# Performance work log

Measured on AMD Instinct MI355X. Metric: run time of the kernel, lower is better.

The kernel has to match this reference:

```python
import jax, jax.numpy as jnp
import numpy as np

HEAD_SIZE = 64

def setup_inputs() -> dict:
    key = jax.random.key(0)
    k1, k2, k3, k4 = jax.random.split(key, 4)
    B, T, C = 4, 4096, 768
    s = 1.0 / np.sqrt(C)
    return {
        "x": jax.random.normal(k1, (B, T, C), dtype=jnp.float32),
        "Wq": jax.random.normal(k2, (C, HEAD_SIZE), dtype=jnp.float32) * s,
        "Wk": jax.random.normal(k3, (C, HEAD_SIZE), dtype=jnp.float32) * s,
        "Wv": jax.random.normal(k4, (C, HEAD_SIZE), dtype=jnp.float32) * s,
    }

def reference(x, Wq, Wk, Wv):
    # x: [B,T,C]; Wq/Wk/Wv: [C,H]
    T = x.shape[1]
    q = jnp.einsum('btc,ch->bth', x, Wq)
    k = jnp.einsum('btc,ch->bth', x, Wk)
    v = jnp.einsum('btc,ch->bth', x, Wv)
    scale = HEAD_SIZE ** (-0.5)
    wei = jnp.einsum('bth,bsh->bts', q, k) * scale  # [B,T,T]
    causal = jnp.tril(jnp.ones((T, T), dtype=bool))
    wei = jnp.where(causal, wei, -jnp.inf)
    wei = jax.nn.softmax(wei, axis=-1)
    # dropout p=0.0 -> identity
    out = jnp.einsum('bts,bsh->bth', wei, v)  # [B,T,H]
    return out
```

## Files before the change

### kernel.cpp

```cpp
#include <hip/hip_runtime.h>
#include <hip/hip_bf16.h>
#include <stdint.h>

typedef unsigned short u16;
typedef __attribute__((ext_vector_type(8))) __bf16 bf16x8;
typedef __attribute__((ext_vector_type(4))) float f32x4;

#define LOG2E 1.44269504088896340736f

__device__ inline u16 f2bf(float f){
  uint32_t u = __float_as_uint(f);
  u += 0x7FFFu + ((u >> 16) & 1u);
  return (u16)(u >> 16);
}
__device__ inline float bf2f(u16 v){
  return __uint_as_float(((uint32_t)v) << 16);
}

__global__ __launch_bounds__(256) void wt_kernel(const float* __restrict__ Wq,
                                                 const float* __restrict__ Wk,
                                                 const float* __restrict__ Wv,
                                                 u16* __restrict__ wtf){
  int idx = blockIdx.x * 256 + threadIdx.x;
  if (idx >= 192 * 768) return;
  int n = idx / 768, c = idx - n * 768;
  int h = n & 63;
  const float* W = (n < 64) ? Wq : ((n < 128) ? Wk : Wv);
  float v = W[c * 64 + h];
  if (n < 64) v *= 0.125f * LOG2E;
  int f = n >> 4, n16 = n & 15;
  int kstep = c >> 5, quad = (c >> 3) & 3, j = c & 7;
  wtf[(size_t)((f * 24 + kstep) * 64 + quad * 16 + n16) * 8 + j] = f2bf(v);
}

__global__ __launch_bounds__(256) void proj_kernel(const float* __restrict__ x,
                                                   const u16* __restrict__ wtf,
                                                   u16* __restrict__ qs,
                                                   u16* __restrict__ ksf,
                                                   u16* __restrict__ vtf){
  __shared__ u16 At[24 * 64 * 8];
  const int tid = threadIdx.x;
  const int w = tid >> 6, lane = tid & 63;
  const int n16 = lane & 15, quad = lane >> 4;
  const int rt = blockIdx.x * 16;

  const float* xb = x + (size_t)rt * 768;
  float4 t[12];
#pragma unroll
  for (int i = 0; i < 12; ++i)
    t[i] = *(const float4*)(xb + (size_t)(i * 256 + tid) * 4);
#pragma unroll
  for (int i = 0; i < 12; ++i){
    int l = i * 256 + tid;
    int row = l / 192, c4 = l - row * 192;
    int ksn = c4 >> 3, qd = (c4 >> 1) & 3, j0 = (c4 & 1) * 4;
    int idx = ((ksn * 64 + qd * 16 + row) * 8 + j0) ^ ((ksn & 7) << 3);
    union { ushort4 s; u16 e[4]; } pk;
    pk.e[0] = f2bf(t[i].x); pk.e[1] = f2bf(t[i].y);
    pk.e[2] = f2bf(t[i].z); pk.e[3] = f2bf(t[i].w);
    *(ushort4*)&At[idx] = pk.s;
  }
  __syncthreads();

  const f32x4 fz = {0.f, 0.f, 0.f, 0.f};
  f32x4 acc[3];
#pragma unroll
  for (int j = 0; j < 3; ++j) acc[j] = fz;

#pragma unroll
  for (int kst = 0; kst < 24; ++kst){
    const int sw = (kst & 7) << 3;
    bf16x8 a = *(const bf16x8*)&At[((kst * 64 + lane) * 8) ^ sw];
#pragma unroll
    for (int j = 0; j < 3; ++j){
      bf16x8 bfr = *(const bf16x8*)(wtf + (size_t)(((3 * w + j) * 24 + kst) * 64 + lane) * 8);
      acc[j] = __builtin_amdgcn_mfma_f32_16x16x32_bf16(a, bfr, acc[j], 0, 0, 0);
    }
  }
  __syncthreads();

#pragma unroll
  for (int j = 0; j < 3; ++j){
    const int F = 3 * w + j;
    const int s = F >> 2, c0 = (F & 3) * 16;
#pragma unroll
    for (int r = 0; r < 4; ++r){
      u16 val = f2bf(acc[j][r]);
      int row = quad * 4 + r;
      if (s < 2) At[s * 1152 + row * 72 + c0 + n16] = val;
      else       At[2304 + (c0 + n16) * 24 + row]   = val;
    }
  }
  __syncthreads();

  const int bb = rt >> 12, t0 = rt & 4095;
  const int kt = t0 >> 6;
  const int fk = (t0 >> 4) & 3;
  const int half0 = (t0 >> 5) & 1;
  const int qhalf = (t0 >> 4) & 1;
  if (tid < 128){
    int row = tid >> 3, hc = tid & 7;
    uint4 qv = *(const uint4*)&At[row * 72 + hc * 8];
    *(uint4*)(qs + (size_t)(rt + row) * 64 + hc * 8) = qv;
  } else {
    int tt = tid - 128;
    int half = tt >> 6, l2 = tt & 63;
    int nn = l2 & 15, qq = l2 >> 4;
    uint4 kv = *(const uint4*)&At[1152 + nn * 72 + half * 32 + qq * 8];
    size_t off = ((((size_t)(bb * 64 + kt) * 4 + fk) * 2 + half) * 64 + l2) * 8;
    *(uint4*)(ksf + off) = kv;
  }
  if (tid < 128){
    int f = tid >> 5, idx5 = tid & 31;
    int qsel = idx5 >> 4, nn = idx5 & 15;
    int h = f * 16 + nn;
    uint4 vv = *(const uint4*)&At[2304 + h * 24 + qsel * 8];
    int lane2 = (2 * qhalf + qsel) * 16 + nn;
    size_t off = ((((size_t)(bb * 64 + kt) * 4 + f) * 2 + half0) * 64 + lane2) * 8;
    *(uint4*)(vtf + off) = vv;
  }
}

__global__ __launch_bounds__(256) void flash_part(const u16* __restrict__ qs,
                                                  const u16* __restrict__ ksf,
                                                  const u16* __restrict__ vtf,
                                                  u16* __restrict__ Opart,
                                                  float* __restrict__ ml){
  const int b  = blockIdx.x >> 9;
  const int qt = (blockIdx.x >> 4) & 31;
  const int ck = blockIdx.x & 15;
  const int kt0 = ck * 4;
  const int ktmax = 2 * qt + 1;
  if (kt0 > ktmax) return;
  const int kt1 = min(ktmax, kt0 + 3);

  __shared__ u16 Ps[128 * 72];
  const int tid = threadIdx.x;
  const int w = tid >> 6, lane = tid & 63;
  const int n16 = lane & 15, quad = lane >> 4;

  const u16* qb = qs + (size_t)b * 262144;
  const u16* kp = ksf + (size_t)b * 262144 + (size_t)kt0 * 4096 + lane * 8;
  const u16* vp = vtf + (size_t)b * 262144 + (size_t)kt0 * 4096 + lane * 8;

  bf16x8 qA[2][2];
#pragma unroll
  for (int m = 0; m < 2; ++m){
    const size_t qrow = (size_t)(qt * 128 + w * 32 + m * 16 + n16) * 64;
    qA[m][0] = *(const bf16x8*)(qb + qrow + quad * 8);
    qA[m][1] = *(const bf16x8*)(qb + qrow + 32 + quad * 8);
  }

  const f32x4 fz = {0.f, 0.f, 0.f, 0.f};
  f32x4 O[2][4];
  float rs[2][4];
#pragma unroll
  for (int m = 0; m < 2; ++m)
#pragma unroll
    for (int f = 0; f < 4; ++f){ O[m][f] = fz; rs[m][f] = 0.f; }

  bf16x8 kf[8];
#pragma unroll
  for (int i = 0; i < 8; ++i) kf[i] = *(const bf16x8*)(kp + i * 512);

  for (int kt = kt0; kt <= kt1; ++kt){
    bf16x8 vf[8];
#pragma unroll
    for (int i = 0; i < 8; ++i)
      vf[i] = *(const bf16x8*)(vp + (size_t)(kt - kt0) * 4096 + i * 512);

    f32x4 S[2][4];
#pragma unroll
    for (int m = 0; m < 2; ++m)
#pragma unroll
      for (int f = 0; f < 4; ++f){
        f32x4 s = fz;
        s = __builtin_amdgcn_mfma_f32_16x16x32_bf16(qA[m][0], kf[f * 2],     s, 0, 0, 0);
        s = __builtin_amdgcn_mfma_f32_16x16x32_bf16(qA[m][1], kf[f * 2 + 1], s, 0, 0, 0);
        S[m][f] = s;
      }

    if (kt < kt1){
#pragma unroll
      for (int i = 0; i < 8; ++i)
        kf[i] = *(const bf16x8*)(kp + (size_t)(kt - kt0 + 1) * 4096 + i * 512);
    }

    if (kt >= 2 * qt){
#pragma unroll
      for (int m = 0; m < 2; ++m)
#pragma unroll
        for (int f = 0; f < 4; ++f)
#pragma unroll
          for (int r = 0; r < 4; ++r){
            int col = kt * 64 + f * 16 + n16;
            int row = qt * 128 + w * 32 + m * 16 + quad * 4 + r;
            if (col > row) S[m][f][r] = -1e30f;
          }
    }

#pragma unroll
    for (int m = 0; m < 2; ++m)
#pragma unroll
      for (int f = 0; f < 4; ++f)
#pragma unroll
        for (int r = 0; r < 4; ++r){
          float p = __builtin_amdgcn_exp2f(S[m][f][r]);
          S[m][f][r] = p;
          rs[m][r] += p;
        }

#pragma unroll
    for (int m = 0; m < 2; ++m)
#pragma unroll
      for (int f = 0; f < 4; ++f){
        u16* p = &Ps[(w * 32 + m * 16 + quad * 4) * 72 + f * 16 + n16];
        p[0]   = f2bf(S[m][f][0]);
        p[72]  = f2bf(S[m][f][1]);
        p[144] = f2bf(S[m][f][2]);
        p[216] = f2bf(S[m][f][3]);
      }
    bf16x8 pA[2][2];
#pragma unroll
    for (int m = 0; m < 2; ++m){
      pA[m][0] = *(const bf16x8*)&Ps[(w * 32 + m * 16 + n16) * 72 + quad * 8];
      pA[m][1] = *(const bf16x8*)&Ps[(w * 32 + m * 16 + n16) * 72 + 32 + quad * 8];
    }

#pragma unroll
    for (int m = 0; m < 2; ++m)
#pragma unroll
      for (int f = 0; f < 4; ++f){
        O[m][f] = __builtin_amdgcn_mfma_f32_16x16x32_bf16(pA[m][0], vf[f * 2],     O[m][f], 0, 0, 0);
        O[m][f] = __builtin_amdgcn_mfma_f32_16x16x32_bf16(pA[m][1], vf[f * 2 + 1], O[m][f], 0, 0, 0);
      }
  }

#pragma unroll
  for (int m = 0; m < 2; ++m)
#pragma unroll
    for (int r = 0; r < 4; ++r){
#pragma unroll
      for (int off = 1; off < 16; off <<= 1)
        rs[m][r] += __shfl_xor(rs[m][r], off, 16);
    }

  const size_t oidx = (size_t)blockIdx.x * 8192;
#pragma unroll
  for (int m = 0; m < 2; ++m)
#pragma unroll
    for (int f = 0; f < 4; ++f)
#pragma unroll
      for (int r = 0; r < 4; ++r){
        int row_local = w * 32 + m * 16 + quad * 4 + r;
        Opart[oidx + (size_t)row_local * 64 + f * 16 + n16] = f2bf(O[m][f][r]);
      }
  if (n16 == 0){
    float* lp = ml + (size_t)blockIdx.x * 128;
#pragma unroll
    for (int m = 0; m < 2; ++m)
#pragma unroll
      for (int r = 0; r < 4; ++r)
        lp[w * 32 + m * 16 + quad * 4 + r] = rs[m][r];
  }
}

__global__ __launch_bounds__(256) void combine_kernel(const u16* __restrict__ Opart,
                                                      const float* __restrict__ ml,
                                                      float* __restrict__ out){
  const int gid = blockIdx.x * 256 + threadIdx.x;
  const int bq = gid >> 11;
  const int rem = (gid & 2047) * 4;
  const int row = rem >> 6;
  const int qt = bq & 31;
  const int nc = (2 * qt + 5) >> 2;

  float L = 0.f;
  float a0 = 0.f, a1 = 0.f, a2 = 0.f, a3 = 0.f;
  for (int c = 0; c < nc; ++c){
    L += ml[((size_t)bq * 16 + c) * 128 + row];
    const u16* p = Opart + ((size_t)bq * 16 + c) * 8192 + rem;
    uint2 d = *(const uint2*)p;
    a0 += bf2f((u16)(d.x & 0xffffu));
    a1 += bf2f((u16)(d.x >> 16));
    a2 += bf2f((u16)(d.y & 0xffffu));
    a3 += bf2f((u16)(d.y >> 16));
  }
  const float invL = 1.0f / L;
  float4 v = {a0 * invL, a1 * invL, a2 * invL, a3 * invL};
  *(float4*)(out + (size_t)gid * 4) = v;
}

extern "C" void kernel_launch(void* const* d_in, const int* in_sizes, int n_in,
                              void* d_out, int out_size, void* d_ws, size_t ws_size,
                              hipStream_t stream){
  const float* x  = (const float*)d_in[0];
  const float* Wq = (const float*)d_in[1];
  const float* Wk = (const float*)d_in[2];
  const float* Wv = (const float*)d_in[3];
  float* out = (float*)d_out;

  u16* qs  = (u16*)d_ws;
  u16* ksf = qs  + (size_t)16384 * 64;
  u16* vtf = ksf + (size_t)16384 * 64;
  u16* wtf = vtf + (size_t)16384 * 64;
  u16* Opart = wtf + (size_t)192 * 768;
  float* ml = (float*)(Opart + (size_t)2048 * 8192);

  wt_kernel<<<576, 256, 0, stream>>>(Wq, Wk, Wv, wtf);
  proj_kernel<<<1024, 256, 0, stream>>>(x, wtf, qs, ksf, vtf);
  flash_part<<<2048, 256, 0, stream>>>(qs, ksf, vtf, Opart, ml);
  combine_kernel<<<1024, 256, 0, stream>>>(Opart, ml, out);
}
```

Before: 140.8 us.

## Stage K/V tiles through double-buffered LDS via direct global-to-LDS loads

Rather than having every wave load its own copy of the K and V fragments from global memory into registers, the block now cooperatively copies each K/V tile into a double-buffered shared-memory buffer with global_load_lds. The next tile is prefetched while the current one is used. This cuts redundant global traffic across the four waves and frees registers. In exchange it adds LDS reads, about 32KB more shared memory, and a barrier per tile. It also relies on the barrier ordering the async LDS writes, with no explicit vmcnt wait.

New measurement: 139.9 us. Within noise of the previous version (-0.6%).

```diff
diff --git a/kernel.cpp b/kernel.cpp
--- a/kernel.cpp
+++ b/kernel.cpp
@@ -15,6 +15,12 @@
 }
 __device__ inline float bf2f(u16 v){
   return __uint_as_float(((uint32_t)v) << 16);
+}
+
+typedef const __attribute__((address_space(1))) void* gas_t;
+typedef __attribute__((address_space(3))) void* las_t;
+__device__ inline void gl_lds16(const void* g, void* l){
+  __builtin_amdgcn_global_load_lds((gas_t)g, (las_t)l, 16, 0, 0);
 }
 
 __global__ __launch_bounds__(256) void wt_kernel(const float* __restrict__ Wq,
@@ -132,16 +138,18 @@
   const int kt0 = ck * 4;
   const int ktmax = 2 * qt + 1;
   if (kt0 > ktmax) return;
-  const int kt1 = min(ktmax, kt0 + 3);
-
+  const int nt = min(ktmax, kt0 + 3) - kt0 + 1;
+
+  __shared__ u16 Kb[2][4096];
+  __shared__ u16 Vb[2][4096];
   __shared__ u16 Ps[128 * 72];
   const int tid = threadIdx.x;
   const int w = tid >> 6, lane = tid & 63;
   const int n16 = lane & 15, quad = lane >> 4;
 
-  const u16* qb = qs + (size_t)b * 262144;
-  const u16* kp = ksf + (size_t)b * 262144 + (size_t)kt0 * 4096 + lane * 8;
-  const u16* vp = vtf + (size_t)b * 262144 + (size_t)kt0 * 4096 + lane * 8;
+  const u16* qb  = qs  + (size_t)b * 262144;
+  const u16* kpg = ksf + (size_t)b * 262144 + (size_t)kt0 * 4096;
+  const u16* vpg = vtf + (size_t)b * 262144 + (size_t)kt0 * 4096;
 
   bf16x8 qA[2][2];
 #pragma unroll
@@ -159,31 +167,36 @@
 #pragma unroll
     for (int f = 0; f < 4; ++f){ O[m][f] = fz; rs[m][f] = 0.f; }
 
-  bf16x8 kf[8];
-#pragma unroll
-  for (int i = 0; i < 8; ++i) kf[i] = *(const bf16x8*)(kp + i * 512);
-
-  for (int kt = kt0; kt <= kt1; ++kt){
-    bf16x8 vf[8];
-#pragma unroll
-    for (int i = 0; i < 8; ++i)
-      vf[i] = *(const bf16x8*)(vp + (size_t)(kt - kt0) * 4096 + i * 512);
+#define STAGE(bf, ti)                                                        \
+  {                                                                          \
+    const u16* kg = kpg + (size_t)(ti) * 4096 + (w * 2) * 512 + lane * 8;    \
+    const u16* vg = vpg + (size_t)(ti) * 4096 + (w * 2) * 512 + lane * 8;    \
+    gl_lds16(kg,       &Kb[bf][(w * 2 + 0) * 512]);                          \
+    gl_lds16(kg + 512, &Kb[bf][(w * 2 + 1) * 512]);                          \
+    gl_lds16(vg,       &Vb[bf][(w * 2 + 0) * 512]);                          \
+    gl_lds16(vg + 512, &Vb[bf][(w * 2 + 1) * 512]);                          \
+  }
+
+  STAGE(0, 0);
+  __syncthreads();
+  int c = 0;
+
+  for (int it = 0; it < nt; ++it){
+    const int kt = kt0 + it;
+    if (it + 1 < nt) STAGE(c ^ 1, it + 1);
 
     f32x4 S[2][4];
 #pragma unroll
-    for (int m = 0; m < 2; ++m)
-#pragma unroll
-      for (int f = 0; f < 4; ++f){
+    for (int f = 0; f < 4; ++f){
+      bf16x8 k0 = *(const bf16x8*)&Kb[c][(f * 2 + 0) * 512 + lane * 8];
+      bf16x8 k1 = *(const bf16x8*)&Kb[c][(f * 2 + 1) * 512 + lane * 8];
+#pragma unroll
+      for (int m = 0; m < 2; ++m){
         f32x4 s = fz;
-        s = __builtin_amdgcn_mfma_f32_16x16x32_bf16(qA[m][0], kf[f * 2],     s, 0, 0, 0);
-        s = __builtin_amdgcn_mfma_f32_16x16x32_bf16(qA[m][1], kf[f * 2 + 1], s, 0, 0, 0);
+        s = __builtin_amdgcn_mfma_f32_16x16x32_bf16(qA[m][0], k0, s, 0, 0, 0);
+        s = __builtin_amdgcn_mfma_f32_16x16x32_bf16(qA[m][1], k1, s, 0, 0, 0);
         S[m][f] = s;
       }
-
-    if (kt < kt1){
-#pragma unroll
-      for (int i = 0; i < 8; ++i)
-        kf[i] = *(const bf16x8*)(kp + (size_t)(kt - kt0 + 1) * 4096 + i * 512);
     }
 
     if (kt >= 2 * qt){
@@ -228,13 +241,20 @@
     }
 
 #pragma unroll
-    for (int m = 0; m < 2; ++m)
-#pragma unroll
-      for (int f = 0; f < 4; ++f){
-        O[m][f] = __builtin_amdgcn_mfma_f32_16x16x32_bf16(pA[m][0], vf[f * 2],     O[m][f], 0, 0, 0);
-        O[m][f] = __builtin_amdgcn_mfma_f32_16x16x32_bf16(pA[m][1], vf[f * 2 + 1], O[m][f], 0, 0, 0);
+    for (int f = 0; f < 4; ++f){
+      bf16x8 v0 = *(const bf16x8*)&Vb[c][(f * 2 + 0) * 512 + lane * 8];
+      bf16x8 v1 = *(const bf16x8*)&Vb[c][(f * 2 + 1) * 512 + lane * 8];
+#pragma unroll
+      for (int m = 0; m < 2; ++m){
+        O[m][f] = __builtin_amdgcn_mfma_f32_16x16x32_bf16(pA[m][0], v0, O[m][f], 0, 0, 0);
+        O[m][f] = __builtin_amdgcn_mfma_f32_16x16x32_bf16(pA[m][1], v1, O[m][f], 0, 0, 0);
       }
-  }
+    }
+
+    __syncthreads();
+    c ^= 1;
+  }
+#undef STAGE
 
 #pragma unroll
   for (int m = 0; m < 2; ++m)
```
